# Optimization experiments

Hardware: AMD Instinct MI355X
Metric: run time of the kernel (lower is better)

Reference implementation:

```python
import jax, jax.numpy as jnp
import numpy as np

N, E, G, D, C = 50000, 800000, 512, 128, 10
BN_EPS = 1e-5

def setup_inputs() -> dict:
    key = jax.random.key(0)
    ks = jax.random.split(key, 12)
    inp = {
        'x': jnp.zeros((N,), dtype=jnp.int64 if jax.config.jax_enable_x64 else jnp.int32),
        'edge_index': jax.random.randint(ks[0], (2, E), 0, N),
        'batch_ids': jnp.sort(jax.random.randint(ks[1], (N,), 0, G)),
        'emb': jax.random.normal(ks[2], (1, D), jnp.float32),
        'W1a': jax.random.normal(ks[3], (D, D), jnp.float32) * 0.05,
        'b1a': jnp.zeros((D,), jnp.float32),
        'g1': jnp.ones((D,), jnp.float32),
        'be1': jnp.zeros((D,), jnp.float32),
        'W1b': jax.random.normal(ks[4], (D, D), jnp.float32) * 0.05,
        'b1b': jnp.zeros((D,), jnp.float32),
        'W2a': jax.random.normal(ks[5], (D, D), jnp.float32) * 0.05,
        'b2a': jnp.zeros((D,), jnp.float32),
        'g2': jnp.ones((D,), jnp.float32),
        'be2': jnp.zeros((D,), jnp.float32),
        'W2b': jax.random.normal(ks[6], (D, D), jnp.float32) * 0.05,
        'b2b': jnp.zeros((D,), jnp.float32),
        'Wm': jax.random.normal(ks[7], (D, C), jnp.float32) * 0.05,
        'bm': jnp.zeros((C,), jnp.float32),
        'Wx': jax.random.normal(ks[8], (D, C), jnp.float32) * 0.05,
        'bx': jnp.zeros((C,), jnp.float32),
        'ens_w': jnp.array([0.6, 0.4], jnp.float32),
    }
    return inp

def _gin_layer(h, src, dst, Wa, ba, g, be, Wb, bb):
    # GINConv, eps=0: mlp(x + sum_{j in N(i)} x_j)
    agg = jax.ops.segment_sum(h[src], dst, num_segments=N)  # [N, D]
    z = (h + agg) @ Wa + ba
    mu = jnp.mean(z, axis=0)
    var = jnp.var(z, axis=0)  # biased, as torch BN training forward
    z = (z - mu) * jax.lax.rsqrt(var + BN_EPS) * g + be
    z = jax.nn.relu(z)  # dropout is identity in eval
    return z @ Wb + bb

def reference(x, edge_index, batch_ids, emb, W1a, b1a, g1, be1, W1b, b1b,
              W2a, b2a, g2, be2, W2b, b2b, Wm, bm, Wx, bx, ens_w):
    src, dst = edge_index[0], edge_index[1]
    h0 = emb[x]  # [N, D] (all indices 0)
    h1 = _gin_layer(h0, src, dst, W1a, b1a, g1, be1, W1b, b1b)
    h2 = _gin_layer(h1, src, dst, W2a, b2a, g2, be2, W2b, b2b) + h1
    # global mean / max pooling over batch segments
    counts = jax.ops.segment_sum(jnp.ones((N,), h2.dtype), batch_ids, num_segments=G)
    mean_repr = jax.ops.segment_sum(h2, batch_ids, num_segments=G) / jnp.maximum(counts, 1.0)[:, None]
    max_repr = jax.ops.segment_max(h2, batch_ids, num_segments=G)
    max_repr = jnp.where(jnp.isfinite(max_repr), max_repr, 0.0)  # empty segments -> 0
    logits_mean = mean_repr @ Wm + bm
    logits_max = max_repr @ Wx + bx
    w = jax.nn.softmax(ens_w)
    ensemble_logits = w[0] * logits_mean + w[1] * logits_max
    return (ensemble_logits, logits_mean, logits_max, (mean_repr, max_repr))
```

## Files before the change

kernel.cpp:

```cpp
#include <hip/hip_runtime.h>
#include <math.h>

#define N_NODES  50000
#define N_EDGES  800000
#define N_GRAPHS 512
#define DIM      128
#define NCLS     10
#define KH       64
#define KW       32
#define KT       128
#define OVF_CAP  65536
#define BN_EPS   1e-5f

#define TR       32
#define NB_GEMM  ((N_NODES + TR - 1) / TR)
#define NB_DEG   32
#define FIN_A    96


__global__ void k_zero(uint4* __restrict__ p, long long n4) {
    long long i = (long long)blockIdx.x * blockDim.x + threadIdx.x;
    if (i < n4) p[i] = make_uint4(0u, 0u, 0u, 0u);
}

__global__ void k_count_deg(const int4* __restrict__ dst4, int* __restrict__ deg) {
    int e = blockIdx.x * blockDim.x + threadIdx.x;
    if (e < N_EDGES / 4) {
        int4 d = dst4[e];
        atomicAdd(&deg[d.x], 1);
        atomicAdd(&deg[d.y], 1);
        atomicAdd(&deg[d.z], 1);
        atomicAdd(&deg[d.w], 1);
    }
}

__device__ inline int lower_bound_i(const int* __restrict__ a, int n, int v) {
    int lo = 0, hi = n;
    while (lo < hi) {
        int mid = (lo + hi) >> 1;
        if (a[mid] < v) lo = mid + 1; else hi = mid;
    }
    return lo;
}

__global__ __launch_bounds__(1024) void k_sumdeg2(
        const int* __restrict__ deg, unsigned long long* __restrict__ dpart,
        const int* __restrict__ batch, int* __restrict__ seg) {
    __shared__ unsigned long long lds[1024];
    const int t = threadIdx.x;
    if (blockIdx.x == 0) {
        if (t < N_GRAPHS) seg[t] = lower_bound_i(batch, N_NODES, t);
        if (t == 0) seg[N_GRAPHS] = N_NODES;
    }
    unsigned long long s = 0;
    for (int i = blockIdx.x * 1024 + t; i < N_NODES; i += NB_DEG * 1024) {
        unsigned long long d = (unsigned long long)(unsigned int)deg[i];
        s += d * d;
    }
    lds[t] = s;
    __syncthreads();
    for (int st = 512; st > 0; st >>= 1) {
        if (t < st) lds[t] += lds[t + st];
        __syncthreads();
    }
    if (t == 0) dpart[blockIdx.x] = lds[0];
}

__global__ void k_tables(const unsigned long long* __restrict__ dpart,
                         const float* __restrict__ emb, const float* __restrict__ W1a,
                         const float* __restrict__ g1, const float* __restrict__ be1,
                         const float* __restrict__ W1b, const float* __restrict__ b1b,
                         const float* __restrict__ W2a,
                         float* __restrict__ table, float* __restrict__ table2) {
    int k = blockIdx.x, d = threadIdx.x;
    __shared__ float r[DIM];
    __shared__ float t[DIM];
    float u = 0.f;
    for (int j = 0; j < DIM; ++j) u += emb[j] * W1a[j * DIM + d];
    unsigned long long s2 = 0;
    #pragma unroll 8
    for (int b = 0; b < NB_DEG; ++b) s2 += dpart[b];
    double mdeg = (double)N_EDGES / (double)N_NODES;
    double vdeg = (double)s2 / (double)N_NODES - mdeg * mdeg;
    float var = (float)((double)u * (double)u * vdeg);
    float rs  = rsqrtf(var + BN_EPS);
    float A   = u * rs * g1[d];
    float B   = be1[d] - (float)mdeg * A;
    float kf = (float)k;
    r[d] = fmaxf(kf * A + B, 0.f);
    __syncthreads();
    float acc = b1b[d];
    for (int j = 0; j < DIM; ++j) acc += r[j] * W1b[j * DIM + d];
    table[(size_t)k * DIM + d] = acc;
    t[d] = acc;
    __syncthreads();
    float acc2 = 0.f;
    for (int j = 0; j < DIM; ++j) acc2 += t[j] * W2a[j * DIM + d];
    table2[(size_t)k * DIM + d] = acc2;
}

__global__ void k_edges(const int4* __restrict__ src4, const int4* __restrict__ dst4,
                        const int* __restrict__ deg, unsigned int* __restrict__ m,
                        unsigned int* __restrict__ ovf_cnt, int* __restrict__ ovf_buf) {
    int e = blockIdx.x * blockDim.x + threadIdx.x;
    if (e >= N_EDGES / 4) return;
    int4 sv = src4[e];
    int4 dv = dst4[e];
    int ss[4] = {sv.x, sv.y, sv.z, sv.w};
    int dd[4] = {dv.x, dv.y, dv.z, dv.w};
    #pragma unroll
    for (int j = 0; j < 4; ++j) {
        int k = deg[ss[j]];
        if (k < KH) {
            atomicAdd(&m[(size_t)dd[j] * KW + (k >> 1)], 1u << ((k & 1) << 4));
        } else {
            unsigned int idx = atomicAdd(ovf_cnt, 1u);
            if (idx < OVF_CAP) {
                ovf_buf[2 * idx] = dd[j];
                ovf_buf[2 * idx + 1] = k;
            }
        }
    }
}

__global__ __launch_bounds__(256) void k_gemm1s(
        const unsigned int* __restrict__ m, const int* __restrict__ deg,
        const float* __restrict__ table2, const float* __restrict__ b2a,
        float* __restrict__ spart,
        const unsigned int* __restrict__ ovf_cnt, const int* __restrict__ ovf_buf) {
    __shared__ __align__(16) unsigned int lds_m[TR * 33];
    __shared__ float red[2048];
    const int t = threadIdx.x;
    const int i0 = blockIdx.x * TR;
    {
        int row = t >> 3, c = (t & 7) << 2;
        uint4 v = make_uint4(0u, 0u, 0u, 0u);
        if (i0 + row < N_NODES) v = *(const uint4*)&m[(size_t)(i0 + row) * KW + c];
        lds_m[row * 33 + c + 0] = v.x;
        lds_m[row * 33 + c + 1] = v.y;
        lds_m[row * 33 + c + 2] = v.z;
        lds_m[row * 33 + c + 3] = v.w;
    }
    __syncthreads();

    const int g = t >> 5;
    const int c4 = (t & 31) << 2;
    const int rbase = g * 4;
    float acc[4][4] = {};
    #pragma unroll 4
    for (int w = 0; w < KW; ++w) {
        float4 ta = *(const float4*)&table2[(size_t)(2 * w) * DIM + c4];
        float4 tb = *(const float4*)&table2[(size_t)(2 * w + 1) * DIM + c4];
        #pragma unroll
        for (int r = 0; r < 4; ++r) {
            unsigned int mw = lds_m[(rbase + r) * 33 + w];
            float lo = (float)(mw & 0xFFFFu);
            float hi = (float)(mw >> 16);
            acc[r][0] += lo * ta.x + hi * tb.x;
            acc[r][1] += lo * ta.y + hi * tb.y;
            acc[r][2] += lo * ta.z + hi * tb.z;
            acc[r][3] += lo * ta.w + hi * tb.w;
        }
    }
    unsigned int nov = *ovf_cnt;
    if (nov > OVF_CAP) nov = OVF_CAP;
    for (unsigned int u = 0; u < nov; ++u) {
        int dd = ovf_buf[2 * u];
        int r = dd - i0;
        if (r >= 0 && r < TR && (r >> 2) == g) {
            int kk = ovf_buf[2 * u + 1]; if (kk > KT - 1) kk = KT - 1;
            float4 tv = *(const float4*)&table2[(size_t)kk * DIM + c4];
            acc[r & 3][0] += tv.x; acc[r & 3][1] += tv.y;
            acc[r & 3][2] += tv.z; acc[r & 3][3] += tv.w;
        }
    }

    float4 bb = *(const float4*)&b2a[c4];
    float s4[4] = {0.f, 0.f, 0.f, 0.f};
    float q4[4] = {0.f, 0.f, 0.f, 0.f};
    #pragma unroll
    for (int r = 0; r < 4; ++r) {
        int row = i0 + rbase + r;
        if (row < N_NODES) {
            int kk = deg[row]; if (kk > KT - 1) kk = KT - 1;
            float4 self = *(const float4*)&table2[(size_t)kk * DIM + c4];
            float v0 = acc[r][0] + self.x + bb.x;
            float v1 = acc[r][1] + self.y + bb.y;
            float v2 = acc[r][2] + self.z + bb.z;
            float v3 = acc[r][3] + self.w + bb.w;
            s4[0] += v0; q4[0] += v0 * v0;
            s4[1] += v1; q4[1] += v1 * v1;
            s4[2] += v2; q4[2] += v2 * v2;
            s4[3] += v3; q4[3] += v3 * v3;
        }
    }
    #pragma unroll
    for (int j = 0; j < 4; ++j) {
        red[g * 128 + c4 + j] = s4[j];
        red[1024 + g * 128 + c4 + j] = q4[j];
    }
    __syncthreads();
    if (t < 128) {
        float ss = 0.f, qq = 0.f;
        #pragma unroll
        for (int gg = 0; gg < 8; ++gg) {
            ss += red[gg * 128 + t];
            qq += red[1024 + gg * 128 + t];
        }
        spart[(size_t)blockIdx.x * 256 + t] = ss;
        spart[(size_t)blockIdx.x * 256 + 128 + t] = qq;
    }
}

__global__ __launch_bounds__(256) void k_fin2a(
        const float* __restrict__ spart, double* __restrict__ spart2) {
    const int t = threadIdx.x;
    double s = 0.0;
    for (int r = blockIdx.x; r < NB_GEMM; r += FIN_A)
        s += (double)spart[(size_t)r * 256 + t];
    spart2[(size_t)blockIdx.x * 256 + t] = s;
}

__global__ __launch_bounds__(256) void k_fin2b(
        const double* __restrict__ spart2,
        const float* __restrict__ g2, const float* __restrict__ be2,
        float* __restrict__ A2, float* __restrict__ B2) {
    __shared__ double red[256];
    const int t = threadIdx.x;
    double s = 0.0;
    #pragma unroll 8
    for (int b = 0; b < FIN_A; ++b) s += spart2[(size_t)b * 256 + t];
    red[t] = s;
    __syncthreads();
    if (t < 128) {
        double mu = red[t] / (double)N_NODES;
        double var = red[128 + t] / (double)N_NODES - mu * mu;
        float rs = rsqrtf((float)var + BN_EPS);
        float a = rs * g2[t];
        A2[t] = a;
        B2[t] = be2[t] - (float)mu * a;
    }
}

__global__ __launch_bounds__(256) void k_gemm2(
        const unsigned int* __restrict__ m, const int* __restrict__ deg,
        const float* __restrict__ table2, const float* __restrict__ b2a,
        const float* __restrict__ A2, const float* __restrict__ B2,
        const float* __restrict__ W2b, const float* __restrict__ b2b,
        const float* __restrict__ table, float* __restrict__ h2,
        const unsigned int* __restrict__ ovf_cnt, const int* __restrict__ ovf_buf) {
    __shared__ __align__(16) unsigned int lds_m[TR * 33];
    __shared__ __align__(16) float lds_zn[TR * 132];
    const int t = threadIdx.x;
    const int i0 = blockIdx.x * TR;
    {
        int row = t >> 3, c = (t & 7) << 2;
        uint4 v = make_uint4(0u, 0u, 0u, 0u);
        if (i0 + row < N_NODES) v = *(const uint4*)&m[(size_t)(i0 + row) * KW + c];
        lds_m[row * 33 + c + 0] = v.x;
        lds_m[row * 33 + c + 1] = v.y;
        lds_m[row * 33 + c + 2] = v.z;
        lds_m[row * 33 + c + 3] = v.w;
    }
    __syncthreads();

    const int g = t >> 5;
    const int c4 = (t & 31) << 2;
    const int rbase = g * 4;
    float acc[4][4] = {};
    #pragma unroll 4
    for (int w = 0; w < KW; ++w) {
        float4 ta = *(const float4*)&table2[(size_t)(2 * w) * DIM + c4];
        float4 tb = *(const float4*)&table2[(size_t)(2 * w + 1) * DIM + c4];
        #pragma unroll
        for (int r = 0; r < 4; ++r) {
            unsigned int mw = lds_m[(rbase + r) * 33 + w];
            float lo = (float)(mw & 0xFFFFu);
            float hi = (float)(mw >> 16);
            acc[r][0] += lo * ta.x + hi * tb.x;
            acc[r][1] += lo * ta.y + hi * tb.y;
            acc[r][2] += lo * ta.z + hi * tb.z;
            acc[r][3] += lo * ta.w + hi * tb.w;
        }
    }
    unsigned int nov = *ovf_cnt;
    if (nov > OVF_CAP) nov = OVF_CAP;
    for (unsigned int u = 0; u < nov; ++u) {
        int dd = ovf_buf[2 * u];
        int r = dd - i0;
        if (r >= 0 && r < TR && (r >> 2) == g) {
            int kk = ovf_buf[2 * u + 1]; if (kk > KT - 1) kk = KT - 1;
            float4 tv = *(const float4*)&table2[(size_t)kk * DIM + c4];
            acc[r & 3][0] += tv.x; acc[r & 3][1] += tv.y;
            acc[r & 3][2] += tv.z; acc[r & 3][3] += tv.w;
        }
    }

    float4 bb = *(const float4*)&b2a[c4];
    float4 av = *(const float4*)&A2[c4];
    float4 bv = *(const float4*)&B2[c4];
    int kks[4];
    #pragma unroll
    for (int r = 0; r < 4; ++r) {
        int row = i0 + rbase + r;
        float z0 = 0.f, z1 = 0.f, z2v = 0.f, z3 = 0.f;
        kks[r] = 0;
        if (row < N_NODES) {
            int kk = deg[row]; if (kk > KT - 1) kk = KT - 1;
            kks[r] = kk;
            float4 self = *(const float4*)&table2[(size_t)kk * DIM + c4];
            z0 = fmaxf((acc[r][0] + self.x + bb.x) * av.x + bv.x, 0.f);
            z1 = fmaxf((acc[r][1] + self.y + bb.y) * av.y + bv.y, 0.f);
            z2v = fmaxf((acc[r][2] + self.z + bb.z) * av.z + bv.z, 0.f);
            z3 = fmaxf((acc[r][3] + self.w + bb.w) * av.w + bv.w, 0.f);
        }
        lds_zn[(rbase + r) * 132 + c4 + 0] = z0;
        lds_zn[(rbase + r) * 132 + c4 + 1] = z1;
        lds_zn[(rbase + r) * 132 + c4 + 2] = z2v;
        lds_zn[(rbase + r) * 132 + c4 + 3] = z3;
    }
    __syncthreads();

    float acc2[4][4] = {};
    #pragma unroll 2
    for (int kb = 0; kb < 32; ++kb) {
        const int k0 = kb * 4;
        float4 w0 = *(const float4*)&W2b[(size_t)(k0 + 0) * DIM + c4];
        float4 w1 = *(const float4*)&W2b[(size_t)(k0 + 1) * DIM + c4];
        float4 w2 = *(const float4*)&W2b[(size_t)(k0 + 2) * DIM + c4];
        float4 w3 = *(const float4*)&W2b[(size_t)(k0 + 3) * DIM + c4];
        #pragma unroll
        for (int r = 0; r < 4; ++r) {
            float4 zr = *(const float4*)&lds_zn[(rbase + r) * 132 + k0];
            acc2[r][0] += zr.x * w0.x + zr.y * w1.x + zr.z * w2.x + zr.w * w3.x;
            acc2[r][1] += zr.x * w0.y + zr.y * w1.y + zr.z * w2.y + zr.w * w3.y;
            acc2[r][2] += zr.x * w0.z + zr.y * w1.z + zr.z * w2.z + zr.w * w3.z;
            acc2[r][3] += zr.x * w0.w + zr.y * w1.w + zr.z * w2.w + zr.w * w3.w;
        }
    }

    float4 bbv = *(const float4*)&b2b[c4];
    #pragma unroll
    for (int r = 0; r < 4; ++r) {
        int row = i0 + rbase + r;
        if (row < N_NODES) {
            float4 tb = *(const float4*)&table[(size_t)kks[r] * DIM + c4];
            float4 o;
            o.x = acc2[r][0] + bbv.x + tb.x;
            o.y = acc2[r][1] + bbv.y + tb.y;
            o.z = acc2[r][2] + bbv.z + tb.z;
            o.w = acc2[r][3] + bbv.w + tb.w;
            *(float4*)&h2[(size_t)row * DIM + c4] = o;
        }
    }
}

__global__ __launch_bounds__(1024) void k_poolhead(
        const float* __restrict__ h2, const int* __restrict__ seg,
        const float* __restrict__ Wm, const float* __restrict__ bm,
        const float* __restrict__ Wx, const float* __restrict__ bx,
        const float* __restrict__ ensw,
        float* __restrict__ out_ens, float* __restrict__ out_lm,
        float* __restrict__ out_lx,
        float* __restrict__ out_mean, float* __restrict__ out_max) {
    __shared__ float reds[32 * 132];
    __shared__ float redm[32 * 132];
    int g = blockIdx.x;
    int s0 = seg[g], e0 = seg[g + 1];
    int rg = threadIdx.x >> 5;
    int c4 = (threadIdx.x & 31) << 2;
    float s[4] = {0.f, 0.f, 0.f, 0.f};
    float mx[4] = {-INFINITY, -INFINITY, -INFINITY, -INFINITY};
    for (int i = s0 + rg; i < e0; i += 32) {
        float4 v = *(const float4*)&h2[(size_t)i * DIM + c4];
        s[0] += v.x; mx[0] = fmaxf(mx[0], v.x);
        s[1] += v.y; mx[1] = fmaxf(mx[1], v.y);
        s[2] += v.z; mx[2] = fmaxf(mx[2], v.z);
        s[3] += v.w; mx[3] = fmaxf(mx[3], v.w);
    }
    #pragma unroll
    for (int j = 0; j < 4; ++j) {
        reds[rg * 132 + c4 + j] = s[j];
        redm[rg * 132 + c4 + j] = mx[j];
    }
    __syncthreads();
    for (int step = 16; step >= 1; step >>= 1) {
        if (rg < step) {
            #pragma unroll
            for (int j = 0; j < 4; ++j) {
                reds[rg * 132 + c4 + j] += reds[(rg + step) * 132 + c4 + j];
                redm[rg * 132 + c4 + j] = fmaxf(redm[rg * 132 + c4 + j],
                                                redm[(rg + step) * 132 + c4 + j]);
            }
        }
        __syncthreads();
    }
    if (rg == 0) {
        int cnt = e0 - s0;
        float denom = (float)(cnt > 0 ? cnt : 1);
        #pragma unroll
        for (int j = 0; j < 4; ++j) {
            float mean = reds[c4 + j] / denom;
            float mxv  = (cnt > 0) ? redm[c4 + j] : 0.f;
            out_mean[(size_t)g * DIM + c4 + j] = mean;
            out_max[(size_t)g * DIM + c4 + j]  = mxv;
            reds[c4 + j] = mean;
            redm[c4 + j] = mxv;
        }
    }
    __syncthreads();
    int t = threadIdx.x;
    if (t < NCLS) {
        float lm = bm[t], lx = bx[t];
        for (int d = 0; d < DIM; ++d) {
            lm += reds[d] * Wm[d * NCLS + t];
            lx += redm[d] * Wx[d * NCLS + t];
        }
        float a0 = ensw[0], a1 = ensw[1];
        float mw = fmaxf(a0, a1);
        float e0v = expf(a0 - mw), e1v = expf(a1 - mw);
        float inv = 1.f / (e0v + e1v);
        out_lm[(size_t)g * NCLS + t] = lm;
        out_lx[(size_t)g * NCLS + t] = lx;
        out_ens[(size_t)g * NCLS + t] = (e0v * inv) * lm + (e1v * inv) * lx;
    }
}


extern "C" void kernel_launch(void* const* d_in, const int* in_sizes, int n_in,
                              void* d_out, int out_size, void* d_ws, size_t ws_size,
                              hipStream_t stream) {
    const int* edge = (const int*)d_in[1];
    const int* src = edge;
    const int* dst = edge + N_EDGES;
    const int* batch = (const int*)d_in[2];
    const float* emb = (const float*)d_in[3];
    const float* W1a = (const float*)d_in[4];
    const float* g1  = (const float*)d_in[6];
    const float* be1 = (const float*)d_in[7];
    const float* W1b = (const float*)d_in[8];
    const float* b1b = (const float*)d_in[9];
    const float* W2a = (const float*)d_in[10];
    const float* b2a = (const float*)d_in[11];
    const float* g2  = (const float*)d_in[12];
    const float* be2 = (const float*)d_in[13];
    const float* W2b = (const float*)d_in[14];
    const float* b2b = (const float*)d_in[15];
    const float* Wm  = (const float*)d_in[16];
    const float* bm  = (const float*)d_in[17];
    const float* Wx  = (const float*)d_in[18];
    const float* bx  = (const float*)d_in[19];
    const float* ensw = (const float*)d_in[20];

    char* ws = (char*)d_ws;
    size_t off = 0;
    auto take = [&](size_t bytes) {
        char* p = ws + off;
        off += (bytes + 511) & ~(size_t)511;
        return p;
    };
    int* deg                  = (int*)take((size_t)N_NODES * 4);
    unsigned int* m           = (unsigned int*)take((size_t)N_NODES * KW * 4);
    unsigned int* ovf_cnt     = (unsigned int*)take(4);
    size_t zbytes = off;
    unsigned long long* dpart = (unsigned long long*)take((size_t)NB_DEG * 8);
    float* spart              = (float*)take((size_t)NB_GEMM * 256 * 4);
    double* spart2            = (double*)take((size_t)FIN_A * 256 * 8);
    int* ovf_buf              = (int*)take((size_t)OVF_CAP * 2 * 4);
    float* table              = (float*)take((size_t)KT * DIM * 4);
    float* table2             = (float*)take((size_t)KT * DIM * 4);
    float* A2                 = (float*)take(DIM * 4);
    float* B2                 = (float*)take(DIM * 4);
    int* seg                  = (int*)take((size_t)(N_GRAPHS + 1) * 4);
    float* h2                 = (float*)take((size_t)N_NODES * DIM * 4);
    (void)ws_size; (void)in_sizes; (void)n_in; (void)out_size;

    float* out      = (float*)d_out;
    float* out_ens  = out;
    float* out_lm   = out + (size_t)N_GRAPHS * NCLS;
    float* out_lx   = out + 2 * (size_t)N_GRAPHS * NCLS;
    float* out_mean = out + 3 * (size_t)N_GRAPHS * NCLS;
    float* out_max  = out_mean + (size_t)N_GRAPHS * DIM;

    long long n4 = (long long)(zbytes >> 4);
    k_zero<<<(int)((n4 + 255) / 256), 256, 0, stream>>>((uint4*)ws, n4);
    k_count_deg<<<(N_EDGES / 4 + 255) / 256, 256, 0, stream>>>((const int4*)dst, deg);
    k_sumdeg2<<<NB_DEG, 1024, 0, stream>>>(deg, dpart, batch, seg);
    k_tables<<<KT, DIM, 0, stream>>>(dpart, emb, W1a, g1, be1, W1b, b1b, W2a,
                                     table, table2);
    k_edges<<<(N_EDGES / 4 + 255) / 256, 256, 0, stream>>>(
        (const int4*)src, (const int4*)dst, deg, m, ovf_cnt, ovf_buf);
    k_gemm1s<<<NB_GEMM, 256, 0, stream>>>(m, deg, table2, b2a, spart, ovf_cnt, ovf_buf);
    k_fin2a<<<FIN_A, 256, 0, stream>>>(spart, spart2);
    k_fin2b<<<1, 256, 0, stream>>>(spart2, g2, be2, A2, B2);
    k_gemm2<<<NB_GEMM, 256, 0, stream>>>(m, deg, table2, b2a, A2, B2, W2b, b2b,
                                         table, h2, ovf_cnt, ovf_buf);
    k_poolhead<<<N_GRAPHS, 1024, 0, stream>>>(h2, seg, Wm, bm, Wx, bx, ensw,
                                              out_ens, out_lm, out_lx, out_mean, out_max);
}
```

Measured before the change: 196.6 us.

## Compute layer-2 BN statistics via degree-histogram Gram matrix instead of full pass

Replaces the first GEMM pass, which computed per-channel sums and sums of squares over all nodes, with a 64x64 Gram matrix of per-node neighbor-degree histograms (plus the self-degree term). Per-channel mean and variance are then derived algebraically from that Gram matrix and the degree-to-feature table, with a serial correction for overflow entries. The main GEMM tile is also doubled to 64 rows per block to improve reuse of table and weight loads. This adds several small kernels and a single-thread overflow loop, and the larger tile raises register pressure.

```diff
diff --git a/kernel.cpp b/kernel.cpp
--- a/kernel.cpp
+++ b/kernel.cpp
@@ -12,10 +12,12 @@
 #define OVF_CAP  65536
 #define BN_EPS   1e-5f
 
-#define TR       32
+#define TR       64
 #define NB_GEMM  ((N_NODES + TR - 1) / TR)
 #define NB_DEG   32
-#define FIN_A    96
+#define GRAM_B   256
+#define GT       64
+#define GRAM_T   4
 
 
 __global__ void k_zero(uint4* __restrict__ p, long long n4) {
@@ -117,128 +119,174 @@
             unsigned int idx = atomicAdd(ovf_cnt, 1u);
             if (idx < OVF_CAP) {
                 ovf_buf[2 * idx] = dd[j];
-                ovf_buf[2 * idx + 1] = k;
+                ovf_buf[2 * idx + 1] = k < KT ? k : KT - 1;
             }
         }
     }
 }
 
-__global__ __launch_bounds__(256) void k_gemm1s(
+__global__ __launch_bounds__(256) void k_gram(
         const unsigned int* __restrict__ m, const int* __restrict__ deg,
+        float* __restrict__ gpart, float* __restrict__ hpart,
+        unsigned int* __restrict__ ovfn_cnt, int* __restrict__ ovfn_buf) {
+    __shared__ float n[GT][68];
+    const int t = threadIdx.x;
+    const int j = t & 63, kq = t >> 6;
+    float acc[16] = {};
+    float hacc = 0.f;
+    for (int tile = 0; tile < GRAM_T; ++tile) {
+        int nbase = (blockIdx.x * GRAM_T + tile) * GT;
+        if (nbase >= N_NODES) break;
+        {
+            int row = t >> 2;
+            int w8 = (t & 3) << 3;
+            uint4 v0 = make_uint4(0u,0u,0u,0u), v1 = make_uint4(0u,0u,0u,0u);
+            if (nbase + row < N_NODES) {
+                v0 = *(const uint4*)&m[(size_t)(nbase + row) * KW + w8];
+                v1 = *(const uint4*)&m[(size_t)(nbase + row) * KW + w8 + 4];
+            }
+            float* np = &n[row][w8 << 1];
+            np[0]  = (float)(v0.x & 0xFFFFu); np[1]  = (float)(v0.x >> 16);
+            np[2]  = (float)(v0.y & 0xFFFFu); np[3]  = (float)(v0.y >> 16);
+            np[4]  = (float)(v0.z & 0xFFFFu); np[5]  = (float)(v0.z >> 16);
+            np[6]  = (float)(v0.w & 0xFFFFu); np[7]  = (float)(v0.w >> 16);
+            np[8]  = (float)(v1.x & 0xFFFFu); np[9]  = (float)(v1.x >> 16);
+            np[10] = (float)(v1.y & 0xFFFFu); np[11] = (float)(v1.y >> 16);
+            np[12] = (float)(v1.z & 0xFFFFu); np[13] = (float)(v1.z >> 16);
+            np[14] = (float)(v1.w & 0xFFFFu); np[15] = (float)(v1.w >> 16);
+        }
+        __syncthreads();
+        if (t < GT) {
+            int i = nbase + t;
+            if (i < N_NODES) {
+                int d = deg[i];
+                if (d < KH) n[t][d] += 1.f;
+                else {
+                    unsigned int idx = atomicAdd(ovfn_cnt, 1u);
+                    if (idx < OVF_CAP) {
+                        ovfn_buf[2 * idx] = i;
+                        ovfn_buf[2 * idx + 1] = d < KT ? d : KT - 1;
+                    }
+                }
+            }
+        }
+        __syncthreads();
+        #pragma unroll 2
+        for (int i = 0; i < GT; ++i) {
+            float a = n[i][j];
+            const float* nk = &n[i][kq << 4];
+            float4 b0 = *(const float4*)&nk[0];
+            float4 b1 = *(const float4*)&nk[4];
+            float4 b2 = *(const float4*)&nk[8];
+            float4 b3 = *(const float4*)&nk[12];
+            acc[0]  += a * b0.x; acc[1]  += a * b0.y; acc[2]  += a * b0.z; acc[3]  += a * b0.w;
+            acc[4]  += a * b1.x; acc[5]  += a * b1.y; acc[6]  += a * b1.z; acc[7]  += a * b1.w;
+            acc[8]  += a * b2.x; acc[9]  += a * b2.y; acc[10] += a * b2.z; acc[11] += a * b2.w;
+            acc[12] += a * b3.x; acc[13] += a * b3.y; acc[14] += a * b3.z; acc[15] += a * b3.w;
+            hacc += a;
+        }
+        __syncthreads();
+    }
+    float* gp = &gpart[(size_t)blockIdx.x * 4096 + j * 64 + (kq << 4)];
+    *(float4*)&gp[0]  = make_float4(acc[0],  acc[1],  acc[2],  acc[3]);
+    *(float4*)&gp[4]  = make_float4(acc[4],  acc[5],  acc[6],  acc[7]);
+    *(float4*)&gp[8]  = make_float4(acc[8],  acc[9],  acc[10], acc[11]);
+    *(float4*)&gp[12] = make_float4(acc[12], acc[13], acc[14], acc[15]);
+    if (kq == 0) hpart[(size_t)blockIdx.x * 64 + j] = hacc;
+}
+
+__global__ __launch_bounds__(256) void k_gred(
+        const float* __restrict__ gpart, const float* __restrict__ hpart,
+        float* __restrict__ G, float* __restrict__ Haug) {
+    const int t = threadIdx.x;
+    if (blockIdx.x < 16) {
+        int e = blockIdx.x * 256 + t;
+        double s = 0.0;
+        #pragma unroll 8
+        for (int b = 0; b < GRAM_B; ++b) s += (double)gpart[(size_t)b * 4096 + e];
+        G[e] = (float)s;
+    } else {
+        if (t < 64) {
+            double s = 0.0;
+            #pragma unroll 8
+            for (int b = 0; b < GRAM_B; ++b) s += (double)hpart[(size_t)b * 64 + t];
+            Haug[t] = (float)s;
+        }
+    }
+}
+
+__global__ __launch_bounds__(256) void k_bn2(
+        const float* __restrict__ G, const float* __restrict__ Haug,
         const float* __restrict__ table2, const float* __restrict__ b2a,
-        float* __restrict__ spart,
-        const unsigned int* __restrict__ ovf_cnt, const int* __restrict__ ovf_buf) {
-    __shared__ __align__(16) unsigned int lds_m[TR * 33];
-    __shared__ float red[2048];
+        const float* __restrict__ g2, const float* __restrict__ be2,
+        const unsigned int* __restrict__ m, const int* __restrict__ deg,
+        const unsigned int* __restrict__ ovf_cnt, const int* __restrict__ ovf_buf,
+        const unsigned int* __restrict__ ovfn_cnt, const int* __restrict__ ovfn_buf,
+        float* __restrict__ A2, float* __restrict__ B2) {
+    __shared__ float td[KT];
+    __shared__ double red[256];
+    __shared__ double sq_sh, hdot_sh;
+    const int d = blockIdx.x;
     const int t = threadIdx.x;
-    const int i0 = blockIdx.x * TR;
+    if (t < KT) td[t] = table2[(size_t)t * DIM + d];
+    __syncthreads();
     {
-        int row = t >> 3, c = (t & 7) << 2;
-        uint4 v = make_uint4(0u, 0u, 0u, 0u);
-        if (i0 + row < N_NODES) v = *(const uint4*)&m[(size_t)(i0 + row) * KW + c];
-        lds_m[row * 33 + c + 0] = v.x;
-        lds_m[row * 33 + c + 1] = v.y;
-        lds_m[row * 33 + c + 2] = v.z;
-        lds_m[row * 33 + c + 3] = v.w;
-    }
-    __syncthreads();
-
-    const int g = t >> 5;
-    const int c4 = (t & 31) << 2;
-    const int rbase = g * 4;
-    float acc[4][4] = {};
-    #pragma unroll 4
-    for (int w = 0; w < KW; ++w) {
-        float4 ta = *(const float4*)&table2[(size_t)(2 * w) * DIM + c4];
-        float4 tb = *(const float4*)&table2[(size_t)(2 * w + 1) * DIM + c4];
+        int j = t & 63, kq = t >> 6;
+        float tj = td[j];
+        double s = 0.0;
+        const float* gp = &G[j * 64 + (kq << 4)];
         #pragma unroll
-        for (int r = 0; r < 4; ++r) {
-            unsigned int mw = lds_m[(rbase + r) * 33 + w];
-            float lo = (float)(mw & 0xFFFFu);
-            float hi = (float)(mw >> 16);
-            acc[r][0] += lo * ta.x + hi * tb.x;
-            acc[r][1] += lo * ta.y + hi * tb.y;
-            acc[r][2] += lo * ta.z + hi * tb.z;
-            acc[r][3] += lo * ta.w + hi * tb.w;
-        }
-    }
-    unsigned int nov = *ovf_cnt;
-    if (nov > OVF_CAP) nov = OVF_CAP;
-    for (unsigned int u = 0; u < nov; ++u) {
-        int dd = ovf_buf[2 * u];
-        int r = dd - i0;
-        if (r >= 0 && r < TR && (r >> 2) == g) {
-            int kk = ovf_buf[2 * u + 1]; if (kk > KT - 1) kk = KT - 1;
-            float4 tv = *(const float4*)&table2[(size_t)kk * DIM + c4];
-            acc[r & 3][0] += tv.x; acc[r & 3][1] += tv.y;
-            acc[r & 3][2] += tv.z; acc[r & 3][3] += tv.w;
-        }
-    }
-
-    float4 bb = *(const float4*)&b2a[c4];
-    float s4[4] = {0.f, 0.f, 0.f, 0.f};
-    float q4[4] = {0.f, 0.f, 0.f, 0.f};
-    #pragma unroll
-    for (int r = 0; r < 4; ++r) {
-        int row = i0 + rbase + r;
-        if (row < N_NODES) {
-            int kk = deg[row]; if (kk > KT - 1) kk = KT - 1;
-            float4 self = *(const float4*)&table2[(size_t)kk * DIM + c4];
-            float v0 = acc[r][0] + self.x + bb.x;
-            float v1 = acc[r][1] + self.y + bb.y;
-            float v2 = acc[r][2] + self.z + bb.z;
-            float v3 = acc[r][3] + self.w + bb.w;
-            s4[0] += v0; q4[0] += v0 * v0;
-            s4[1] += v1; q4[1] += v1 * v1;
-            s4[2] += v2; q4[2] += v2 * v2;
-            s4[3] += v3; q4[3] += v3 * v3;
-        }
-    }
-    #pragma unroll
-    for (int j = 0; j < 4; ++j) {
-        red[g * 128 + c4 + j] = s4[j];
-        red[1024 + g * 128 + c4 + j] = q4[j];
-    }
-    __syncthreads();
-    if (t < 128) {
-        float ss = 0.f, qq = 0.f;
-        #pragma unroll
-        for (int gg = 0; gg < 8; ++gg) {
-            ss += red[gg * 128 + t];
-            qq += red[1024 + gg * 128 + t];
-        }
-        spart[(size_t)blockIdx.x * 256 + t] = ss;
-        spart[(size_t)blockIdx.x * 256 + 128 + t] = qq;
-    }
-}
-
-__global__ __launch_bounds__(256) void k_fin2a(
-        const float* __restrict__ spart, double* __restrict__ spart2) {
-    const int t = threadIdx.x;
-    double s = 0.0;
-    for (int r = blockIdx.x; r < NB_GEMM; r += FIN_A)
-        s += (double)spart[(size_t)r * 256 + t];
-    spart2[(size_t)blockIdx.x * 256 + t] = s;
-}
-
-__global__ __launch_bounds__(256) void k_fin2b(
-        const double* __restrict__ spart2,
-        const float* __restrict__ g2, const float* __restrict__ be2,
-        float* __restrict__ A2, float* __restrict__ B2) {
-    __shared__ double red[256];
-    const int t = threadIdx.x;
-    double s = 0.0;
-    #pragma unroll 8
-    for (int b = 0; b < FIN_A; ++b) s += spart2[(size_t)b * 256 + t];
-    red[t] = s;
-    __syncthreads();
-    if (t < 128) {
-        double mu = red[t] / (double)N_NODES;
-        double var = red[128 + t] / (double)N_NODES - mu * mu;
+        for (int q = 0; q < 16; ++q)
+            s += (double)gp[q] * (double)(tj * td[(kq << 4) + q]);
+        red[t] = s;
+    }
+    __syncthreads();
+    for (int st = 128; st > 0; st >>= 1) {
+        if (t < st) red[t] += red[t + st];
+        __syncthreads();
+    }
+    if (t == 0) sq_sh = red[0];
+    __syncthreads();
+    red[t] = (t < 64) ? (double)Haug[t] * (double)td[t] : 0.0;
+    __syncthreads();
+    for (int st = 128; st > 0; st >>= 1) {
+        if (t < st) red[t] += red[t + st];
+        __syncthreads();
+    }
+    if (t == 0) hdot_sh = red[0];
+    __syncthreads();
+    if (t == 0) {
+        double b = (double)b2a[d];
+        double hdot = hdot_sh;
+        double sum = hdot + (double)N_NODES * b;
+        double sq  = sq_sh + 2.0 * b * hdot + (double)N_NODES * b * b;
+        unsigned int ne = *ovf_cnt;  if (ne > OVF_CAP) ne = OVF_CAP;
+        unsigned int nn = *ovfn_cnt; if (nn > OVF_CAP) nn = OVF_CAP;
+        for (unsigned int pass = 0; pass < 2; ++pass) {
+            unsigned int cnt = pass == 0 ? ne : nn;
+            const int* buf = pass == 0 ? ovf_buf : ovfn_buf;
+            for (unsigned int u = 0; u < cnt; ++u) {
+                int v  = buf[2 * u];
+                int kk = buf[2 * u + 1];
+                double base = b;
+                for (int w = 0; w < KW; ++w) {
+                    unsigned int mw = m[(size_t)v * KW + w];
+                    base += (double)(mw & 0xFFFFu) * td[2 * w]
+                          + (double)(mw >> 16) * td[2 * w + 1];
+                }
+                int dv = deg[v];
+                if (dv < KH) base += (double)td[dv];
+                double S = (double)td[kk];
+                sum += S;
+                sq  += 2.0 * base * S + S * S;
+            }
+        }
+        double mu = sum / (double)N_NODES;
+        double var = sq / (double)N_NODES - mu * mu;
         float rs = rsqrtf((float)var + BN_EPS);
-        float a = rs * g2[t];
-        A2[t] = a;
-        B2[t] = be2[t] - (float)mu * a;
+        float a = rs * g2[d];
+        A2[d] = a;
+        B2[d] = be2[d] - (float)mu * a;
     }
 }
 
@@ -253,8 +301,10 @@
     __shared__ __align__(16) float lds_zn[TR * 132];
     const int t = threadIdx.x;
     const int i0 = blockIdx.x * TR;
-    {
-        int row = t >> 3, c = (t & 7) << 2;
+    #pragma unroll
+    for (int q = 0; q < 2; ++q) {
+        int idx = t + 256 * q;
+        int row = idx >> 3, c = (idx & 7) << 2;
         uint4 v = make_uint4(0u, 0u, 0u, 0u);
         if (i0 + row < N_NODES) v = *(const uint4*)&m[(size_t)(i0 + row) * KW + c];
         lds_m[row * 33 + c + 0] = v.x;
@@ -266,14 +316,14 @@
 
     const int g = t >> 5;
     const int c4 = (t & 31) << 2;
-    const int rbase = g * 4;
-    float acc[4][4] = {};
+    const int rbase = g * 8;
+    float acc[8][4] = {};
     #pragma unroll 4
     for (int w = 0; w < KW; ++w) {
         float4 ta = *(const float4*)&table2[(size_t)(2 * w) * DIM + c4];
         float4 tb = *(const float4*)&table2[(size_t)(2 * w + 1) * DIM + c4];
         #pragma unroll
-        for (int r = 0; r < 4; ++r) {
+        for (int r = 0; r < 8; ++r) {
             unsigned int mw = lds_m[(rbase + r) * 33 + w];
             float lo = (float)(mw & 0xFFFFu);
             float hi = (float)(mw >> 16);
@@ -287,21 +337,21 @@
     if (nov > OVF_CAP) nov = OVF_CAP;
     for (unsigned int u = 0; u < nov; ++u) {
         int dd = ovf_buf[2 * u];
-        int r = dd - i0;
-        if (r >= 0 && r < TR && (r >> 2) == g) {
-            int kk = ovf_buf[2 * u + 1]; if (kk > KT - 1) kk = KT - 1;
+        int rr = dd - i0;
+        if (rr >= 0 && rr < TR && (rr >> 3) == g) {
+            int kk = ovf_buf[2 * u + 1];
             float4 tv = *(const float4*)&table2[(size_t)kk * DIM + c4];
-            acc[r & 3][0] += tv.x; acc[r & 3][1] += tv.y;
-            acc[r & 3][2] += tv.z; acc[r & 3][3] += tv.w;
+            acc[rr & 7][0] += tv.x; acc[rr & 7][1] += tv.y;
+            acc[rr & 7][2] += tv.z; acc[rr & 7][3] += tv.w;
         }
     }
 
     float4 bb = *(const float4*)&b2a[c4];
     float4 av = *(const float4*)&A2[c4];
     float4 bv = *(const float4*)&B2[c4];
-    int kks[4];
+    int kks[8];
     #pragma unroll
-    for (int r = 0; r < 4; ++r) {
+    for (int r = 0; r < 8; ++r) {
         int row = i0 + rbase + r;
         float z0 = 0.f, z1 = 0.f, z2v = 0.f, z3 = 0.f;
         kks[r] = 0;
@@ -309,10 +359,10 @@
             int kk = deg[row]; if (kk > KT - 1) kk = KT - 1;
             kks[r] = kk;
             float4 self = *(const float4*)&table2[(size_t)kk * DIM + c4];
-            z0 = fmaxf((acc[r][0] + self.x + bb.x) * av.x + bv.x, 0.f);
-            z1 = fmaxf((acc[r][1] + self.y + bb.y) * av.y + bv.y, 0.f);
+            z0  = fmaxf((acc[r][0] + self.x + bb.x) * av.x + bv.x, 0.f);
+            z1  = fmaxf((acc[r][1] + self.y + bb.y) * av.y + bv.y, 0.f);
             z2v = fmaxf((acc[r][2] + self.z + bb.z) * av.z + bv.z, 0.f);
-            z3 = fmaxf((acc[r][3] + self.w + bb.w) * av.w + bv.w, 0.f);
+            z3  = fmaxf((acc[r][3] + self.w + bb.w) * av.w + bv.w, 0.f);
         }
         lds_zn[(rbase + r) * 132 + c4 + 0] = z0;
         lds_zn[(rbase + r) * 132 + c4 + 1] = z1;
@@ -321,7 +371,7 @@
     }
     __syncthreads();
 
-    float acc2[4][4] = {};
+    float acc2[8][4] = {};
     #pragma unroll 2
     for (int kb = 0; kb < 32; ++kb) {
         const int k0 = kb * 4;
@@ -330,7 +380,7 @@
         float4 w2 = *(const float4*)&W2b[(size_t)(k0 + 2) * DIM + c4];
         float4 w3 = *(const float4*)&W2b[(size_t)(k0 + 3) * DIM + c4];
         #pragma unroll
-        for (int r = 0; r < 4; ++r) {
+        for (int r = 0; r < 8; ++r) {
             float4 zr = *(const float4*)&lds_zn[(rbase + r) * 132 + k0];
             acc2[r][0] += zr.x * w0.x + zr.y * w1.x + zr.z * w2.x + zr.w * w3.x;
             acc2[r][1] += zr.x * w0.y + zr.y * w1.y + zr.z * w2.y + zr.w * w3.y;
@@ -341,7 +391,7 @@
 
     float4 bbv = *(const float4*)&b2b[c4];
     #pragma unroll
-    for (int r = 0; r < 4; ++r) {
+    for (int r = 0; r < 8; ++r) {
         int row = i0 + rbase + r;
         if (row < N_NODES) {
             float4 tb = *(const float4*)&table[(size_t)kks[r] * DIM + c4];
@@ -462,11 +512,15 @@
     int* deg                  = (int*)take((size_t)N_NODES * 4);
     unsigned int* m           = (unsigned int*)take((size_t)N_NODES * KW * 4);
     unsigned int* ovf_cnt     = (unsigned int*)take(4);
+    unsigned int* ovfn_cnt    = (unsigned int*)take(4);
     size_t zbytes = off;
     unsigned long long* dpart = (unsigned long long*)take((size_t)NB_DEG * 8);
-    float* spart              = (float*)take((size_t)NB_GEMM * 256 * 4);
-    double* spart2            = (double*)take((size_t)FIN_A * 256 * 8);
+    float* gpart              = (float*)take((size_t)GRAM_B * 4096 * 4);
+    float* hpart              = (float*)take((size_t)GRAM_B * 64 * 4);
+    float* G                  = (float*)take((size_t)4096 * 4);
+    float* Haug               = (float*)take((size_t)64 * 4);
     int* ovf_buf              = (int*)take((size_t)OVF_CAP * 2 * 4);
+    int* ovfn_buf             = (int*)take((size_t)OVF_CAP * 2 * 4);
     float* table              = (float*)take((size_t)KT * DIM * 4);
     float* table2             = (float*)take((size_t)KT * DIM * 4);
     float* A2                 = (float*)take(DIM * 4);
@@ -486,13 +540,14 @@
     k_zero<<<(int)((n4 + 255) / 256), 256, 0, stream>>>((uint4*)ws, n4);
     k_count_deg<<<(N_EDGES / 4 + 255) / 256, 256, 0, stream>>>((const int4*)dst, deg);
     k_sumdeg2<<<NB_DEG, 1024, 0, stream>>>(deg, dpart, batch, seg);
+    k_edges<<<(N_EDGES / 4 + 255) / 256, 256, 0, stream>>>(
+        (const int4*)src, (const int4*)dst, deg, m, ovf_cnt, ovf_buf);
     k_tables<<<KT, DIM, 0, stream>>>(dpart, emb, W1a, g1, be1, W1b, b1b, W2a,
                                      table, table2);
-    k_edges<<<(N_EDGES / 4 + 255) / 256, 256, 0, stream>>>(
-        (const int4*)src, (const int4*)dst, deg, m, ovf_cnt, ovf_buf);
-    k_gemm1s<<<NB_GEMM, 256, 0, stream>>>(m, deg, table2, b2a, spart, ovf_cnt, ovf_buf);
-    k_fin2a<<<FIN_A, 256, 0, stream>>>(spart, spart2);
-    k_fin2b<<<1, 256, 0, stream>>>(spart2, g2, be2, A2, B2);
+    k_gram<<<GRAM_B, 256, 0, stream>>>(m, deg, gpart, hpart, ovfn_cnt, ovfn_buf);
+    k_gred<<<17, 256, 0, stream>>>(gpart, hpart, G, Haug);
+    k_bn2<<<DIM, 256, 0, stream>>>(G, Haug, table2, b2a, g2, be2, m, deg,
+                                   ovf_cnt, ovf_buf, ovfn_cnt, ovfn_buf, A2, B2);
     k_gemm2<<<NB_GEMM, 256, 0, stream>>>(m, deg, table2, b2a, A2, B2, W2b, b2b,
                                          table, h2, ovf_cnt, ovf_buf);
     k_poolhead<<<N_GRAPHS, 1024, 0, stream>>>(h2, seg, Wm, bm, Wx, bx, ensw,
```

After: 210.4 us. +7.0%, slower.
